# Optimization experiments

Hardware: AMD Instinct MI355X
Metric: run time of the kernel (lower is better)

The kernel has to match this reference:

```python
import jax, jax.numpy as jnp
import numpy as np

N_SAMPLES = 16_777_216  # total surviving samples across all rays
N_RAY = 65_536          # number of rays


def setup_inputs() -> dict:
    key = jax.random.key(0)
    k1, k2 = jax.random.split(key)
    alpha = jax.random.uniform(k1, (N_SAMPLES,), dtype=jnp.float32)
    # sorted ray ids -> contiguous segments, as produced by create_full_step_id + masking
    ray_id = jnp.sort(jax.random.randint(k2, (N_SAMPLES,), 0, N_RAY, dtype=jnp.int32))
    return {"alpha": alpha, "ray_id": ray_id, "N_ray": N_RAY}


def _seg_prod_op(a, b):
    # segmented-product combine: reset the running product at segment starts
    va, fa = a
    vb, fb = b
    return jnp.where(fb, vb, va * vb), fa | fb


def reference(alpha, ray_id, N_ray):
    n = alpha.shape[0]
    one_minus_alpha = 1.0 - alpha + 1e-11                      # [n]
    is_start = jnp.concatenate(
        [jnp.ones((1,), jnp.bool_), ray_id[1:] != ray_id[:-1]]
    )                                                          # [n] segment starts
    # parallel segmented cumulative product (replaces the per-sample Python loop)
    cumprod, _ = jax.lax.associative_scan(_seg_prod_op, (one_minus_alpha, is_start))
    # NOTE: faithful to the source: transmittance is a global shift of cumprod
    # (cat([1, cumprod[:-1]])), NOT reset to 1 at each ray start.
    transmittance = jnp.concatenate([jnp.ones((1,), alpha.dtype), cumprod[:-1]])
    weights = alpha * transmittance                            # [n]
    # last sample index of each ray (ids are sorted, so max index == last write)
    last_idx = jnp.zeros((N_ray,), jnp.int32).at[ray_id].max(
        jnp.arange(n, dtype=jnp.int32)
    )                                                          # [N_ray]
    alphainv_last = cumprod[last_idx]                          # [N_ray]
    return weights, alphainv_last
```

## Files before the change

kernel.cpp:

```cpp
#include <hip/hip_runtime.h>
#include <stdint.h>


#define BLOCK 256
#define PER_THREAD 16
#define CHUNK (BLOCK * PER_THREAD)
#define NWAVE (BLOCK / 64)

struct Pair { float v; int f; };

__device__ __forceinline__ Pair seg_combine(Pair a, Pair b) {
    Pair r;
    r.v = b.f ? b.v : (a.v * b.v);
    r.f = a.f | b.f;
    return r;
}

__global__ __launch_bounds__(BLOCK)
void nerf_reduce(const float* __restrict__ alpha, const int* __restrict__ ray_id,
                 float2* __restrict__ agg, float* __restrict__ alphainv,
                 int N_ray, int n) {
    const int c = blockIdx.x;
    const int t = threadIdx.x;
    const long gstart = (long)c * CHUNK + (long)t * PER_THREAD;

    {
        int gid = c * BLOCK + t;
        if (gid < N_ray) alphainv[gid] = (1.0f - alpha[0]) + 1e-11f;
    }

    Pair run; run.v = 1.0f; run.f = 0;
    int prev = (gstart > 0 && gstart < (long)n) ? ray_id[gstart - 1] : -1;
    const bool full = (gstart + PER_THREAD) <= (long)n;

    if (full) {
        #pragma unroll
        for (int q = 0; q < PER_THREAD / 4; ++q) {
            float4 av = *(const float4*)(alpha  + gstart + 4 * q);
            int4   rv = *(const int4*)  (ray_id + gstart + 4 * q);
            float aa[4] = {av.x, av.y, av.z, av.w};
            int   rr[4] = {rv.x, rv.y, rv.z, rv.w};
            #pragma unroll
            for (int j = 0; j < 4; ++j) {
                Pair e; e.v = (1.0f - aa[j]) + 1e-11f; e.f = (rr[j] != prev);
                prev = rr[j];
                run = seg_combine(run, e);
            }
        }
    } else if (gstart < (long)n) {
        for (int k = 0; k < PER_THREAD; ++k) {
            long g = gstart + k;
            if (g < n) {
                int r = ray_id[g];
                Pair e; e.v = (1.0f - alpha[g]) + 1e-11f; e.f = (r != prev);
                prev = r;
                run = seg_combine(run, e);
            }
        }
    }

    #pragma unroll
    for (int off = 1; off < 64; off <<= 1) {
        Pair o;
        o.v = __shfl_down(run.v, off);
        o.f = __shfl_down(run.f, off);
        run = seg_combine(run, o);
    }

    __shared__ float s_wv[NWAVE];
    __shared__ int   s_wf[NWAVE];
    const int lane = t & 63, wid = t >> 6;
    if (lane == 0) { s_wv[wid] = run.v; s_wf[wid] = run.f; }
    __syncthreads();
    if (t == 0) {
        Pair acc; acc.v = s_wv[0]; acc.f = s_wf[0];
        #pragma unroll
        for (int w = 1; w < NWAVE; ++w) {
            Pair e; e.v = s_wv[w]; e.f = s_wf[w];
            acc = seg_combine(acc, e);
        }
        agg[c] = make_float2(acc.v, __int_as_float(acc.f));
    }
}

__global__ void nerf_init_rest(const float* __restrict__ alpha,
                               float* __restrict__ alphainv_tail, int count) {
    int i = blockIdx.x * blockDim.x + threadIdx.x;
    if (i < count) alphainv_tail[i] = (1.0f - alpha[0]) + 1e-11f;
}

__global__ __launch_bounds__(BLOCK)
void nerf_apply(const float* __restrict__ alpha, const int* __restrict__ ray_id,
                const float2* __restrict__ agg,
                float* __restrict__ weights, float* __restrict__ alphainv, int n) {
    __shared__ float s_wv[NWAVE];
    __shared__ int   s_wf[NWAVE];
    __shared__ float s_pv;
    __shared__ int   s_pf;

    const int c = blockIdx.x;
    const int t = threadIdx.x;
    const int lane = t & 63, wid = t >> 6;
    const long gstart = (long)c * CHUNK + (long)t * PER_THREAD;

    float a[PER_THREAD];
    int   rid[PER_THREAD];
    const bool full = (gstart + PER_THREAD) <= (long)n;

    if (full) {
        #pragma unroll
        for (int q = 0; q < PER_THREAD / 4; ++q) {
            float4 av = *(const float4*)(alpha  + gstart + 4 * q);
            int4   rv = *(const int4*)  (ray_id + gstart + 4 * q);
            a[4*q+0] = av.x; a[4*q+1] = av.y; a[4*q+2] = av.z; a[4*q+3] = av.w;
            rid[4*q+0] = rv.x; rid[4*q+1] = rv.y; rid[4*q+2] = rv.z; rid[4*q+3] = rv.w;
        }
    } else {
        #pragma unroll
        for (int k = 0; k < PER_THREAD; ++k) {
            long g = gstart + k;
            a[k]   = (g < n) ? alpha[g]  : 0.0f;
            rid[k] = (g < n) ? ray_id[g] : -2;
        }
    }
    const int prev0 = (gstart > 0 && gstart < (long)n) ? ray_id[gstart - 1] : -1;
    const int rid_next = ((gstart + PER_THREAD) < (long)n) ? ray_id[gstart + PER_THREAD] : -1;

    Pair run; run.v = 1.0f; run.f = 0;
    {
        int prev = prev0;
        #pragma unroll
        for (int k = 0; k < PER_THREAD; ++k) {
            bool inb = (gstart + k) < (long)n;
            Pair e;
            e.v = inb ? ((1.0f - a[k]) + 1e-11f) : 1.0f;
            e.f = inb ? (rid[k] != prev ? 1 : 0) : 0;
            prev = rid[k];
            run = seg_combine(run, e);
        }
    }

    Pair val = run;
    #pragma unroll
    for (int off = 1; off < 64; off <<= 1) {
        Pair o;
        o.v = __shfl_up(val.v, off);
        o.f = __shfl_up(val.f, off);
        if (lane >= off) val = seg_combine(o, val);
    }
    Pair lexcl;
    {
        float ev = __shfl_up(val.v, 1);
        int   ef = __shfl_up(val.f, 1);
        if (lane == 0) { lexcl.v = 1.0f; lexcl.f = 0; }
        else           { lexcl.v = ev;   lexcl.f = ef; }
    }

    if (lane == 63) { s_wv[wid] = val.v; s_wf[wid] = val.f; }

    if (t == 0) {
        Pair pre; pre.v = 1.0f; pre.f = 0;
        for (int j = c - 1; j >= 0; --j) {
            float2 g = agg[j];
            Pair e; e.v = g.x; e.f = __float_as_int(g.y);
            pre = (j == c - 1) ? e : seg_combine(e, pre);
            if (pre.f) break;
        }
        s_pv = pre.v; s_pf = pre.f;
    }
    __syncthreads();

    Pair wexcl; wexcl.v = 1.0f; wexcl.f = 0;
    #pragma unroll
    for (int w = 0; w < NWAVE; ++w) {
        if (w < wid) {
            Pair e; e.v = s_wv[w]; e.f = s_wf[w];
            wexcl = seg_combine(wexcl, e);
        }
    }
    Pair cpre; cpre.v = s_pv; cpre.f = s_pf;
    Pair run2 = seg_combine(seg_combine(cpre, wexcl), lexcl);

    {
        int prev = prev0;
        #pragma unroll
        for (int k = 0; k < PER_THREAD; ++k) {
            bool inb = (gstart + k) < (long)n;
            float om = (1.0f - a[k]) + 1e-11f;
            int   f  = inb ? (rid[k] != prev ? 1 : 0) : 0;
            prev = rid[k];
            float trans = run2.v;
            if (inb) {
                Pair e; e.v = om; e.f = f;
                run2 = seg_combine(run2, e);
            }
            a[k] = a[k] * trans;
            int nxt = (k + 1 < PER_THREAD) ? rid[k + 1] : rid_next;
            if (inb && nxt != rid[k])
                alphainv[rid[k]] = run2.v;
        }
    }

    if (full) {
        #pragma unroll
        for (int q = 0; q < PER_THREAD / 4; ++q) {
            float4 wv;
            wv.x = a[4*q+0]; wv.y = a[4*q+1]; wv.z = a[4*q+2]; wv.w = a[4*q+3];
            *(float4*)(weights + gstart + 4 * q) = wv;
        }
    } else {
        for (int k = 0; k < PER_THREAD; ++k) {
            long g = gstart + k;
            if (g < n) weights[g] = a[k];
        }
    }
}

extern "C" void kernel_launch(void* const* d_in, const int* in_sizes, int n_in,
                              void* d_out, int out_size, void* d_ws, size_t ws_size,
                              hipStream_t stream) {
    const float* alpha  = (const float*)d_in[0];
    const int*   ray_id = (const int*)d_in[1];
    const int n     = in_sizes[0];
    const int N_ray = out_size - n;

    float* weights  = (float*)d_out;
    float* alphainv = weights + n;
    float2* agg     = (float2*)d_ws;

    const int nchunks = (n + CHUNK - 1) / CHUNK;

    nerf_reduce<<<nchunks, BLOCK, 0, stream>>>(alpha, ray_id, agg, alphainv, N_ray, n);
    if (N_ray > nchunks * BLOCK) {
        int extra = N_ray - nchunks * BLOCK;
        nerf_init_rest<<<(extra + BLOCK - 1) / BLOCK, BLOCK, 0, stream>>>(
            alpha, alphainv + nchunks * BLOCK, extra);
    }
    nerf_apply<<<nchunks, BLOCK, 0, stream>>>(alpha, ray_id, agg, weights, alphainv, n);
}
```

Baseline: 192.3 us.

## Double per-thread elements, batch loads upfront, and detect segment ends from the next sample

Raises elements per thread from 16 to 32, which halves the block count and the number of chunk aggregates the serial look-back has to walk. Both kernels now issue all vector loads before any compute to get more memory-level parallelism. The apply kernel writes each ray's alphainv when it meets the next segment's start instead of reading one extra ray_id past the thread's range, and the look-back now overlaps the loads. More registers per thread and the added occupancy hints could lower occupancy.

```diff
diff --git a/kernel.cpp b/kernel.cpp
--- a/kernel.cpp
+++ b/kernel.cpp
@@ -3,8 +3,9 @@
 
 
 #define BLOCK 256
-#define PER_THREAD 16
-#define CHUNK (BLOCK * PER_THREAD)
+#define PT 32
+#define NV (PT / 4)
+#define CHUNK (BLOCK * PT)
 #define NWAVE (BLOCK / 64)
 
 struct Pair { float v; int f; };
@@ -16,13 +17,12 @@
     return r;
 }
 
-__global__ __launch_bounds__(BLOCK)
+__global__ __launch_bounds__(BLOCK, 4)
 void nerf_reduce(const float* __restrict__ alpha, const int* __restrict__ ray_id,
                  float2* __restrict__ agg, float* __restrict__ alphainv,
                  int N_ray, int n) {
-    const int c = blockIdx.x;
-    const int t = threadIdx.x;
-    const long gstart = (long)c * CHUNK + (long)t * PER_THREAD;
+    const int c = blockIdx.x, t = threadIdx.x;
+    const long gstart = (long)c * CHUNK + (long)t * PT;
 
     {
         int gid = c * BLOCK + t;
@@ -30,25 +30,29 @@
     }
 
     Pair run; run.v = 1.0f; run.f = 0;
-    int prev = (gstart > 0 && gstart < (long)n) ? ray_id[gstart - 1] : -1;
-    const bool full = (gstart + PER_THREAD) <= (long)n;
-
-    if (full) {
-        #pragma unroll
-        for (int q = 0; q < PER_THREAD / 4; ++q) {
-            float4 av = *(const float4*)(alpha  + gstart + 4 * q);
-            int4   rv = *(const int4*)  (ray_id + gstart + 4 * q);
-            float aa[4] = {av.x, av.y, av.z, av.w};
-            int   rr[4] = {rv.x, rv.y, rv.z, rv.w};
-            #pragma unroll
-            for (int j = 0; j < 4; ++j) {
-                Pair e; e.v = (1.0f - aa[j]) + 1e-11f; e.f = (rr[j] != prev);
-                prev = rr[j];
-                run = seg_combine(run, e);
-            }
+
+    if (gstart + PT <= (long)n) {
+        float4 AV[NV]; int4 RV[NV];
+        #pragma unroll
+        for (int q = 0; q < NV; ++q) {
+            AV[q] = *(const float4*)(alpha  + gstart + 4 * q);
+            RV[q] = *(const int4*)  (ray_id + gstart + 4 * q);
+        }
+        int prev = (gstart > 0) ? ray_id[gstart - 1] : -1;
+
+        #pragma unroll
+        for (int q = 0; q < NV; ++q) {
+            const float4 av = AV[q]; const int4 rv = RV[q];
+            Pair e;
+            e.v = (1.0f - av.x) + 1e-11f; e.f = (rv.x != prev); run = seg_combine(run, e);
+            e.v = (1.0f - av.y) + 1e-11f; e.f = (rv.y != rv.x); run = seg_combine(run, e);
+            e.v = (1.0f - av.z) + 1e-11f; e.f = (rv.z != rv.y); run = seg_combine(run, e);
+            e.v = (1.0f - av.w) + 1e-11f; e.f = (rv.w != rv.z); run = seg_combine(run, e);
+            prev = rv.w;
         }
     } else if (gstart < (long)n) {
-        for (int k = 0; k < PER_THREAD; ++k) {
+        int prev = (gstart > 0) ? ray_id[gstart - 1] : -1;
+        for (int k = 0; k < PT; ++k) {
             long g = gstart + k;
             if (g < n) {
                 int r = ray_id[g];
@@ -69,14 +73,14 @@
 
     __shared__ float s_wv[NWAVE];
     __shared__ int   s_wf[NWAVE];
-    const int lane = t & 63, wid = t >> 6;
-    if (lane == 0) { s_wv[wid] = run.v; s_wf[wid] = run.f; }
+    const int lane = t & 63, w = t >> 6;
+    if (lane == 0) { s_wv[w] = run.v; s_wf[w] = run.f; }
     __syncthreads();
     if (t == 0) {
         Pair acc; acc.v = s_wv[0]; acc.f = s_wf[0];
         #pragma unroll
-        for (int w = 1; w < NWAVE; ++w) {
-            Pair e; e.v = s_wv[w]; e.f = s_wf[w];
+        for (int ww = 1; ww < NWAVE; ++ww) {
+            Pair e; e.v = s_wv[ww]; e.f = s_wf[ww];
             acc = seg_combine(acc, e);
         }
         agg[c] = make_float2(acc.v, __int_as_float(acc.f));
@@ -89,7 +93,7 @@
     if (i < count) alphainv_tail[i] = (1.0f - alpha[0]) + 1e-11f;
 }
 
-__global__ __launch_bounds__(BLOCK)
+__global__ __launch_bounds__(BLOCK, 3)
 void nerf_apply(const float* __restrict__ alpha, const int* __restrict__ ray_id,
                 const float2* __restrict__ agg,
                 float* __restrict__ weights, float* __restrict__ alphainv, int n) {
@@ -98,65 +102,9 @@
     __shared__ float s_pv;
     __shared__ int   s_pf;
 
-    const int c = blockIdx.x;
-    const int t = threadIdx.x;
-    const int lane = t & 63, wid = t >> 6;
-    const long gstart = (long)c * CHUNK + (long)t * PER_THREAD;
-
-    float a[PER_THREAD];
-    int   rid[PER_THREAD];
-    const bool full = (gstart + PER_THREAD) <= (long)n;
-
-    if (full) {
-        #pragma unroll
-        for (int q = 0; q < PER_THREAD / 4; ++q) {
-            float4 av = *(const float4*)(alpha  + gstart + 4 * q);
-            int4   rv = *(const int4*)  (ray_id + gstart + 4 * q);
-            a[4*q+0] = av.x; a[4*q+1] = av.y; a[4*q+2] = av.z; a[4*q+3] = av.w;
-            rid[4*q+0] = rv.x; rid[4*q+1] = rv.y; rid[4*q+2] = rv.z; rid[4*q+3] = rv.w;
-        }
-    } else {
-        #pragma unroll
-        for (int k = 0; k < PER_THREAD; ++k) {
-            long g = gstart + k;
-            a[k]   = (g < n) ? alpha[g]  : 0.0f;
-            rid[k] = (g < n) ? ray_id[g] : -2;
-        }
-    }
-    const int prev0 = (gstart > 0 && gstart < (long)n) ? ray_id[gstart - 1] : -1;
-    const int rid_next = ((gstart + PER_THREAD) < (long)n) ? ray_id[gstart + PER_THREAD] : -1;
-
-    Pair run; run.v = 1.0f; run.f = 0;
-    {
-        int prev = prev0;
-        #pragma unroll
-        for (int k = 0; k < PER_THREAD; ++k) {
-            bool inb = (gstart + k) < (long)n;
-            Pair e;
-            e.v = inb ? ((1.0f - a[k]) + 1e-11f) : 1.0f;
-            e.f = inb ? (rid[k] != prev ? 1 : 0) : 0;
-            prev = rid[k];
-            run = seg_combine(run, e);
-        }
-    }
-
-    Pair val = run;
-    #pragma unroll
-    for (int off = 1; off < 64; off <<= 1) {
-        Pair o;
-        o.v = __shfl_up(val.v, off);
-        o.f = __shfl_up(val.f, off);
-        if (lane >= off) val = seg_combine(o, val);
-    }
-    Pair lexcl;
-    {
-        float ev = __shfl_up(val.v, 1);
-        int   ef = __shfl_up(val.f, 1);
-        if (lane == 0) { lexcl.v = 1.0f; lexcl.f = 0; }
-        else           { lexcl.v = ev;   lexcl.f = ef; }
-    }
-
-    if (lane == 63) { s_wv[wid] = val.v; s_wf[wid] = val.f; }
+    const int c = blockIdx.x, t = threadIdx.x;
+    const int lane = t & 63, w = t >> 6;
+    const long gstart = (long)c * CHUNK + (long)t * PT;
 
     if (t == 0) {
         Pair pre; pre.v = 1.0f; pre.f = 0;
@@ -168,50 +116,136 @@
         }
         s_pv = pre.v; s_pf = pre.f;
     }
+
+    const bool full = (gstart + PT) <= (long)n;
+    float4 AV[NV]; int4 RV[NV];
+    if (full) {
+        #pragma unroll
+        for (int q = 0; q < NV; ++q) {
+            AV[q] = *(const float4*)(alpha  + gstart + 4 * q);
+            RV[q] = *(const int4*)  (ray_id + gstart + 4 * q);
+        }
+    } else {
+        #pragma unroll
+        for (int q = 0; q < NV; ++q) {
+            float aa[4]; int rr[4];
+            #pragma unroll
+            for (int k = 0; k < 4; ++k) {
+                long g = gstart + 4 * q + k;
+                aa[k] = (g < n) ? alpha[g]  : 0.0f;
+                rr[k] = (g < n) ? ray_id[g] : -2;
+            }
+            AV[q] = make_float4(aa[0], aa[1], aa[2], aa[3]);
+            RV[q] = make_int4(rr[0], rr[1], rr[2], rr[3]);
+        }
+    }
+    const int prev0 = (gstart > 0 && gstart < (long)n) ? ray_id[gstart - 1] : -1;
+
+    Pair loc; loc.v = 1.0f; loc.f = 0;
+    {
+        int prev = prev0;
+        #pragma unroll
+        for (int q = 0; q < NV; ++q) {
+            const float4 av = AV[q]; const int4 rv = RV[q];
+            if (full) {
+                Pair e;
+                e.v = (1.0f - av.x) + 1e-11f; e.f = (rv.x != prev); loc = seg_combine(loc, e);
+                e.v = (1.0f - av.y) + 1e-11f; e.f = (rv.y != rv.x); loc = seg_combine(loc, e);
+                e.v = (1.0f - av.z) + 1e-11f; e.f = (rv.z != rv.y); loc = seg_combine(loc, e);
+                e.v = (1.0f - av.w) + 1e-11f; e.f = (rv.w != rv.z); loc = seg_combine(loc, e);
+                prev = rv.w;
+            } else {
+                const float aa[4] = {av.x, av.y, av.z, av.w};
+                const int   rr[4] = {rv.x, rv.y, rv.z, rv.w};
+                #pragma unroll
+                for (int k = 0; k < 4; ++k) {
+                    long g = gstart + 4 * q + k;
+                    if (g < n) {
+                        Pair e; e.v = (1.0f - aa[k]) + 1e-11f; e.f = (rr[k] != prev);
+                        prev = rr[k];
+                        loc = seg_combine(loc, e);
+                    }
+                }
+            }
+        }
+    }
+
+    Pair inc = loc;
+    #pragma unroll
+    for (int off = 1; off < 64; off <<= 1) {
+        Pair o;
+        o.v = __shfl_up(inc.v, off);
+        o.f = __shfl_up(inc.f, off);
+        if (lane >= off) inc = seg_combine(o, inc);
+    }
+    Pair lexcl;
+    {
+        float uv = __shfl_up(inc.v, 1);
+        int   uf = __shfl_up(inc.f, 1);
+        if (lane == 0) { lexcl.v = 1.0f; lexcl.f = 0; }
+        else           { lexcl.v = uv;   lexcl.f = uf; }
+    }
+    if (lane == 63) { s_wv[w] = inc.v; s_wf[w] = inc.f; }
     __syncthreads();
 
-    Pair wexcl; wexcl.v = 1.0f; wexcl.f = 0;
+    Pair base; base.v = s_pv; base.f = s_pf;
     #pragma unroll
-    for (int w = 0; w < NWAVE; ++w) {
-        if (w < wid) {
-            Pair e; e.v = s_wv[w]; e.f = s_wf[w];
-            wexcl = seg_combine(wexcl, e);
-        }
-    }
-    Pair cpre; cpre.v = s_pv; cpre.f = s_pf;
-    Pair run2 = seg_combine(seg_combine(cpre, wexcl), lexcl);
-
-    {
-        int prev = prev0;
-        #pragma unroll
-        for (int k = 0; k < PER_THREAD; ++k) {
-            bool inb = (gstart + k) < (long)n;
-            float om = (1.0f - a[k]) + 1e-11f;
-            int   f  = inb ? (rid[k] != prev ? 1 : 0) : 0;
-            prev = rid[k];
-            float trans = run2.v;
-            if (inb) {
-                Pair e; e.v = om; e.f = f;
-                run2 = seg_combine(run2, e);
-            }
-            a[k] = a[k] * trans;
-            int nxt = (k + 1 < PER_THREAD) ? rid[k + 1] : rid_next;
-            if (inb && nxt != rid[k])
-                alphainv[rid[k]] = run2.v;
-        }
-    }
-
-    if (full) {
-        #pragma unroll
-        for (int q = 0; q < PER_THREAD / 4; ++q) {
-            float4 wv;
-            wv.x = a[4*q+0]; wv.y = a[4*q+1]; wv.z = a[4*q+2]; wv.w = a[4*q+3];
-            *(float4*)(weights + gstart + 4 * q) = wv;
-        }
-    } else {
-        for (int k = 0; k < PER_THREAD; ++k) {
-            long g = gstart + k;
-            if (g < n) weights[g] = a[k];
+    for (int ww = 0; ww < NWAVE; ++ww) {
+        if (ww < w) {
+            Pair e; e.v = s_wv[ww]; e.f = s_wf[ww];
+            base = seg_combine(base, e);
+        }
+    }
+    Pair P = seg_combine(base, lexcl);
+
+    {
+        int prevRid = prev0;
+        #pragma unroll
+        for (int q = 0; q < NV; ++q) {
+            const float4 av = AV[q]; const int4 rv = RV[q];
+            const long e0 = gstart + 4 * q;
+            if (full) {
+                float w0, w1, w2, w3;
+                int f = (rv.x != prevRid);
+                w0 = av.x * P.v;
+                if (f && e0 > 0) alphainv[prevRid] = P.v;
+                { Pair e; e.v = (1.0f - av.x) + 1e-11f; e.f = f; P = seg_combine(P, e); }
+                if (e0 == (long)n - 1) alphainv[rv.x] = P.v;
+                f = (rv.y != rv.x);
+                w1 = av.y * P.v;
+                if (f) alphainv[rv.x] = P.v;
+                { Pair e; e.v = (1.0f - av.y) + 1e-11f; e.f = f; P = seg_combine(P, e); }
+                if (e0 + 1 == (long)n - 1) alphainv[rv.y] = P.v;
+                f = (rv.z != rv.y);
+                w2 = av.z * P.v;
+                if (f) alphainv[rv.y] = P.v;
+                { Pair e; e.v = (1.0f - av.z) + 1e-11f; e.f = f; P = seg_combine(P, e); }
+                if (e0 + 2 == (long)n - 1) alphainv[rv.z] = P.v;
+                f = (rv.w != rv.z);
+                w3 = av.w * P.v;
+                if (f) alphainv[rv.z] = P.v;
+                { Pair e; e.v = (1.0f - av.w) + 1e-11f; e.f = f; P = seg_combine(P, e); }
+                if (e0 + 3 == (long)n - 1) alphainv[rv.w] = P.v;
+
+                *(float4*)(weights + e0) = make_float4(w0, w1, w2, w3);
+            } else {
+                const float aa[4] = {av.x, av.y, av.z, av.w};
+                const int   rr[4] = {rv.x, rv.y, rv.z, rv.w};
+                #pragma unroll
+                for (int k = 0; k < 4; ++k) {
+                    long g = e0 + k;
+                    if (g < n) {
+                        int f = (rr[k] != prevRid);
+                        float wv = aa[k] * P.v;
+                        if (f && g > 0) alphainv[prevRid] = P.v;
+                        { Pair e; e.v = (1.0f - aa[k]) + 1e-11f; e.f = f; P = seg_combine(P, e); }
+                        if (g == (long)n - 1) alphainv[rr[k]] = P.v;
+                        weights[g] = wv;
+                        prevRid = rr[k];
+                    }
+                }
+            }
+            if (full) prevRid = rv.w;
         }
     }
 }
```

Measured after the change: 211.0 us. 9.7% more time.
